# Performance work log

Hardware: AMD Instinct MI355X
Metric: run time of the kernel (lower is better)

## Reference

```python
import jax, jax.numpy as jnp
import numpy as np

HIDDEN = 1024
NUM_HEADS = 16
HEAD_DIM = HIDDEN // NUM_HEADS
B, S = 2, 2048


def setup_inputs() -> dict:
    key = jax.random.key(0)
    ks = jax.random.split(key, 7)
    scale = 1.0 / np.sqrt(HIDDEN)
    return {
        "hidden_states": jax.random.normal(ks[0], (B, S, HIDDEN), dtype=jnp.float32),
        "attention_mask": jnp.ones((B, S), dtype=jnp.float32),
        "Wq": jax.random.normal(ks[1], (HIDDEN, HIDDEN), dtype=jnp.float32) * scale,
        "bq": jax.random.normal(ks[2], (HIDDEN,), dtype=jnp.float32) * 0.02,
        "Wk": jax.random.normal(ks[3], (HIDDEN, HIDDEN), dtype=jnp.float32) * scale,
        "bk": jax.random.normal(ks[4], (HIDDEN,), dtype=jnp.float32) * 0.02,
        "Wv": jax.random.normal(ks[5], (HIDDEN, HIDDEN), dtype=jnp.float32) * scale,
        "bv": jax.random.normal(ks[6], (HIDDEN,), dtype=jnp.float32) * 0.02,
    }


def reference(hidden_states, attention_mask, Wq, bq, Wk, bk, Wv, bv):
    # Linear projections (W stored [in, out], equivalent to torch Linear).
    q = hidden_states @ Wq + bq  # [B,S,H]
    k = hidden_states @ Wk + bk
    v = hidden_states @ Wv + bv

    def split_heads(x):  # [B,S,H] -> [B,nh,S,hd]
        return x.reshape(B, S, NUM_HEADS, HEAD_DIM).transpose(0, 2, 1, 3)

    q, k, v = split_heads(q), split_heads(k), split_heads(v)

    scores = jnp.einsum("bhqd,bhkd->bhqk", q, k) / jnp.sqrt(
        jnp.asarray(HEAD_DIM, dtype=q.dtype))
    min_val = jnp.finfo(scores.dtype).min
    ext_mask = (1.0 - attention_mask[:, None, None, :]) * min_val  # [B,1,1,S]
    scores = scores + ext_mask
    probs = jax.nn.softmax(scores, axis=-1)  # eval mode: no dropout
    ctx = jnp.einsum("bhqk,bhkd->bhqd", probs, v)
    ctx = ctx.transpose(0, 2, 1, 3).reshape(B, S, HIDDEN)
    return ctx
```

## Files before the change

### kernel.cpp

```cpp
#include <hip/hip_runtime.h>
#include <hip/hip_bf16.h>
#include <cstddef>
#include <cstdint>

#define HID 1024
#define NHEADS 16
#define HDIM 64
#define BATCH 2
#define SEQ 2048
#define MROWS (BATCH * SEQ)
#define BHT (BATCH * NHEADS)

typedef __attribute__((ext_vector_type(8))) short s8v;
typedef __attribute__((ext_vector_type(4))) float f4v;
typedef __attribute__((ext_vector_type(2))) unsigned int u2v;

__device__ __forceinline__ unsigned int pkbf(float a, float b) {
    __hip_bfloat162 h = __float22bfloat162_rn(float2{a, b});
    union { __hip_bfloat162 v; unsigned int u; } c; c.v = h; return c.u;
}

__device__ __forceinline__ void lds_load16(void* lds, const void* g) {
    __builtin_amdgcn_global_load_lds(
        (const __attribute__((address_space(1))) void*)g,
        (__attribute__((address_space(3))) void*)lds, 16, 0, 0);
}

__global__ __launch_bounds__(256) void conv_fused_kernel(
    const float* __restrict__ hs, const float* __restrict__ mask,
    const float* __restrict__ Wq, const float* __restrict__ Wk,
    const float* __restrict__ Wv,
    unsigned short* __restrict__ Ah, unsigned short* __restrict__ WTh,
    float* __restrict__ lmask)
{
    if (blockIdx.x < 2048) {
        const int idx = (blockIdx.x * 256 + threadIdx.x) * 8;
        float4 v0 = *(const float4*)&hs[idx];
        float4 v1 = *(const float4*)&hs[idx + 4];
        union { unsigned int w[4]; } pk;
        pk.w[0] = pkbf(v0.x, v0.y);
        pk.w[1] = pkbf(v0.z, v0.w);
        pk.w[2] = pkbf(v1.x, v1.y);
        pk.w[3] = pkbf(v1.z, v1.w);
        *(uint4*)&Ah[idx] = *(uint4*)&pk;
    } else if (blockIdx.x < 2816) {
        const int bid = blockIdx.x - 2048;
        const int z = bid >> 8;
        const int rem = bid & 255;
        const float* W = (z == 0) ? Wq : (z == 1) ? Wk : Wv;
        unsigned short* th = WTh + (size_t)z * HID * HID;

        __shared__ float tile[64][65];
        const int t = threadIdx.x;
        const int kb = (rem >> 4) * 64, nb = (rem & 15) * 64;
        const int c4 = (t & 15) * 4;
        const int r0 = t >> 4;

#pragma unroll
        for (int i = 0; i < 4; ++i) {
            int r = r0 + i * 16;
            float4 v = *(const float4*)&W[(size_t)(kb + r) * HID + nb + c4];
            tile[r][c4 + 0] = v.x; tile[r][c4 + 1] = v.y;
            tile[r][c4 + 2] = v.z; tile[r][c4 + 3] = v.w;
        }
        __syncthreads();
#pragma unroll
        for (int i = 0; i < 4; ++i) {
            int n = r0 + i * 16;
            union { unsigned int w[2]; unsigned long long q; } pk;
            pk.w[0] = pkbf(tile[c4 + 0][n], tile[c4 + 1][n]);
            pk.w[1] = pkbf(tile[c4 + 2][n], tile[c4 + 3][n]);
            *(unsigned long long*)&th[(size_t)(nb + n) * HID + kb + c4] = pk.q;
        }
    } else {
        const int idx = (blockIdx.x - 2816) * 256 + threadIdx.x;
        lmask[idx] = (mask[idx] - 1.0f) * 1e30f;
    }
}

#define QSCALE 0.18033688011112042f

__global__ __launch_bounds__(256, 2) void qkv_mfma_kernel(
    const unsigned short* __restrict__ Ah, const unsigned short* __restrict__ WTh,
    const float* __restrict__ bq, const float* __restrict__ bk,
    const float* __restrict__ bv,
    unsigned short* __restrict__ Qg, unsigned short* __restrict__ Khi,
    unsigned short* __restrict__ VTg)
{
    __shared__ unsigned short S[24576];
    unsigned short* AS = S;
    unsigned short* B0 = S + 8192;
    unsigned short* B1 = S + 16384;

    const int z2 = blockIdx.z;
    const int t = threadIdx.x;
    const int wave = t >> 6, lane = t & 63, quad = lane >> 4, l15 = lane & 15;
    const int sw = l15 & 7;
    const int wm = wave >> 1, wn = wave & 1;
    const int rowBase = blockIdx.x * 128;
    const int colBase = blockIdx.y * 128;

    const int srow8 = lane >> 3;
    const int sc    = lane & 7;

    const unsigned short* BhQ = WTh;
    const unsigned short* BhK = WTh + (size_t)HID * HID;
    const unsigned short* BhV = WTh + (size_t)2 * HID * HID;

    size_t goffA[4], goffB[4];
#pragma unroll
    for (int it = 0; it < 4; ++it) {
        const int row = (wave * 4 + it) * 8 + srow8;
        const int gx = (sc ^ (row & 7)) * 8;
        goffA[it] = (size_t)(rowBase + row) * HID + gx;
        goffB[it] = (size_t)(colBase + row) * HID + gx;
    }

    if (z2 == 0) {
        f4v accq[4][4], acck[4][4];
#pragma unroll
        for (int mf = 0; mf < 4; ++mf)
#pragma unroll
            for (int nf = 0; nf < 4; ++nf) {
                accq[mf][nf] = (f4v){0.f, 0.f, 0.f, 0.f};
                acck[mf][nf] = (f4v){0.f, 0.f, 0.f, 0.f};
            }

        for (int kt = 0; kt < HID / 64; ++kt) {
            const int k0 = kt * 64;
            __syncthreads();
#pragma unroll
            for (int it = 0; it < 4; ++it) {
                lds_load16(&AS[(wave * 4 + it) * 512], &Ah[goffA[it] + k0]);
                lds_load16(&B0[(wave * 4 + it) * 512], &BhQ[goffB[it] + k0]);
                lds_load16(&B1[(wave * 4 + it) * 512], &BhK[goffB[it] + k0]);
            }
            __syncthreads();

#pragma unroll
            for (int kk = 0; kk < 2; ++kk) {
                const int csw = ((kk * 4 + quad) ^ sw) * 8;
                s8v af[4], bfq[4], bfk[4];
#pragma unroll
                for (int mf = 0; mf < 4; ++mf)
                    af[mf] = *(const s8v*)&AS[(wm * 64 + mf * 16 + l15) * 64 + csw];
#pragma unroll
                for (int nf = 0; nf < 4; ++nf) {
                    bfq[nf] = *(const s8v*)&B0[(wn * 64 + nf * 16 + l15) * 64 + csw];
                    bfk[nf] = *(const s8v*)&B1[(wn * 64 + nf * 16 + l15) * 64 + csw];
                }
#pragma unroll
                for (int mf = 0; mf < 4; ++mf)
#pragma unroll
                    for (int nf = 0; nf < 4; ++nf) {
                        accq[mf][nf] = __builtin_amdgcn_mfma_f32_16x16x32_bf16(bfq[nf], af[mf], accq[mf][nf], 0, 0, 0);
                        acck[mf][nf] = __builtin_amdgcn_mfma_f32_16x16x32_bf16(bfk[nf], af[mf], acck[mf][nf], 0, 0, 0);
                    }
            }
        }

#pragma unroll
        for (int nf = 0; nf < 4; ++nf) {
            const int n0 = colBase + wn * 64 + nf * 16 + quad * 4;
            const float4 bbq = *(const float4*)&bq[n0];
            const float4 bbk = *(const float4*)&bk[n0];
            const int h = n0 >> 6, d0 = n0 & 63;
#pragma unroll
            for (int mf = 0; mf < 4; ++mf) {
                const int rw = rowBase + wm * 64 + mf * 16 + l15;
                const int b = rw >> 11;
                const int ss = rw & (SEQ - 1);
                const size_t base = ((size_t)(b * NHEADS + h) * SEQ + ss) * HDIM + d0;
                union { unsigned int w[2]; unsigned long long q; } pk;
                pk.w[0] = pkbf((accq[mf][nf][0] + bbq.x) * QSCALE, (accq[mf][nf][1] + bbq.y) * QSCALE);
                pk.w[1] = pkbf((accq[mf][nf][2] + bbq.z) * QSCALE, (accq[mf][nf][3] + bbq.w) * QSCALE);
                *(unsigned long long*)&Qg[base] = pk.q;
                pk.w[0] = pkbf(acck[mf][nf][0] + bbk.x, acck[mf][nf][1] + bbk.y);
                pk.w[1] = pkbf(acck[mf][nf][2] + bbk.z, acck[mf][nf][3] + bbk.w);
                *(unsigned long long*)&Khi[base] = pk.q;
            }
        }
    } else {
        f4v acc[4][4];
#pragma unroll
        for (int mf = 0; mf < 4; ++mf)
#pragma unroll
            for (int nf = 0; nf < 4; ++nf) acc[mf][nf] = (f4v){0.f, 0.f, 0.f, 0.f};

        for (int kt = 0; kt < HID / 64; ++kt) {
            const int k0 = kt * 64;
            __syncthreads();
#pragma unroll
            for (int it = 0; it < 4; ++it) {
                lds_load16(&AS[(wave * 4 + it) * 512], &Ah[goffA[it] + k0]);
                lds_load16(&B0[(wave * 4 + it) * 512], &BhV[goffB[it] + k0]);
            }
            __syncthreads();

#pragma unroll
            for (int kk = 0; kk < 2; ++kk) {
                const int csw = ((kk * 4 + quad) ^ sw) * 8;
                s8v af[4], bf[4];
#pragma unroll
                for (int mf = 0; mf < 4; ++mf)
                    af[mf] = *(const s8v*)&AS[(wm * 64 + mf * 16 + l15) * 64 + csw];
#pragma unroll
                for (int nf = 0; nf < 4; ++nf)
                    bf[nf] = *(const s8v*)&B0[(wn * 64 + nf * 16 + l15) * 64 + csw];
#pragma unroll
                for (int mf = 0; mf < 4; ++mf)
#pragma unroll
                    for (int nf = 0; nf < 4; ++nf)
                        acc[mf][nf] = __builtin_amdgcn_mfma_f32_16x16x32_bf16(af[mf], bf[nf], acc[mf][nf], 0, 0, 0);
            }
        }

#pragma unroll
        for (int nf = 0; nf < 4; ++nf) {
            const int n = colBase + wn * 64 + nf * 16 + l15;
            const float bb = bv[n];
            const int h = n >> 6, d = n & 63;
#pragma unroll
            for (int mf = 0; mf < 4; ++mf) {
                const int rw0 = rowBase + wm * 64 + mf * 16 + quad * 4;
                const int b = rw0 >> 11;
                const int s0 = rw0 & (SEQ - 1);
                union { unsigned int w[2]; unsigned long long q; } pk;
                pk.w[0] = pkbf(acc[mf][nf][0] + bb, acc[mf][nf][1] + bb);
                pk.w[1] = pkbf(acc[mf][nf][2] + bb, acc[mf][nf][3] + bb);
                *(unsigned long long*)&VTg[((size_t)(b * NHEADS + h) * HDIM + d) * SEQ + s0] = pk.q;
            }
        }
    }
}

#define BC 64
#define NT (SEQ / BC)

#define ATTN_STEP(KT, KCUR, KNXT, VCUR, VPRV, PAOUT, PAIN, STAGEK, DOPV)      \
    do {                                                                      \
        if (STAGEK)                                                           \
            lds_load16((KNXT) + wave * 512,                                   \
                       kbase + ((KT) + 1) * BC * HDIM + koff);                \
        lds_load16((VCUR) + wave * 512, vbase + (KT) * BC + voff);            \
        float4 msv[4];                                                        \
        _Pragma("unroll") for (int mf = 0; mf < 4; ++mf)                      \
            msv[mf] = *(const float4*)&mrow[(KT) * BC + mf * 16 + quad * 4];  \
        f4v sacc[4];                                                          \
        _Pragma("unroll") for (int mf = 0; mf < 4; ++mf)                      \
            sacc[mf] = (f4v){msv[mf].x, msv[mf].y, msv[mf].z, msv[mf].w};     \
        __builtin_amdgcn_s_setprio(1);                                        \
        _Pragma("unroll") for (int mf = 0; mf < 4; ++mf) {                    \
            _Pragma("unroll") for (int ds = 0; ds < 2; ++ds) {                \
                s8v kh = *(const s8v*)&(KCUR)[(mf * 16 + l15) * HDIM +        \
                                              (((ds * 4 + quad) ^ sw) * 8)];  \
                sacc[mf] = __builtin_amdgcn_mfma_f32_16x16x32_bf16(           \
                    kh, qh[ds], sacc[mf], 0, 0, 0);                           \
            }                                                                 \
        }                                                                     \
        __builtin_amdgcn_s_setprio(0);                                        \
        unsigned int wlo[4], whi[4];                                          \
        float ps = 0.f;                                                       \
        _Pragma("unroll") for (int mf = 0; mf < 4; ++mf) {                    \
            float e0 = __builtin_amdgcn_exp2f(sacc[mf][0]);                   \
            float e1 = __builtin_amdgcn_exp2f(sacc[mf][1]);                   \
            float e2 = __builtin_amdgcn_exp2f(sacc[mf][2]);                   \
            float e3 = __builtin_amdgcn_exp2f(sacc[mf][3]);                   \
            ps += (e0 + e1) + (e2 + e3);                                      \
            wlo[mf] = pkbf(e0, e1);                                           \
            whi[mf] = pkbf(e2, e3);                                           \
        }                                                                     \
        l_r += ps;                                                            \
        _Pragma("unroll") for (int ks = 0; ks < 2; ++ks) {                    \
            unsigned int alo = wlo[ks * 2], blo = wlo[ks * 2 + 1];            \
            unsigned int ahi = whi[ks * 2], bhi = whi[ks * 2 + 1];            \
            u2v r;                                                            \
            r = __builtin_amdgcn_permlane32_swap(alo, blo, false, false);     \
            alo = r[0]; blo = r[1];                                           \
            r = __builtin_amdgcn_permlane32_swap(ahi, bhi, false, false);     \
            ahi = r[0]; bhi = r[1];                                           \
            r = __builtin_amdgcn_permlane16_swap(alo, blo, false, false);     \
            alo = r[0]; blo = r[1];                                           \
            r = __builtin_amdgcn_permlane16_swap(ahi, bhi, false, false);     \
            ahi = r[0]; bhi = r[1];                                           \
            union { unsigned int w[4]; s8v v; } up;                           \
            up.w[0] = alo; up.w[1] = ahi; up.w[2] = blo; up.w[3] = bhi;       \
            PAOUT[ks] = up.v;                                                 \
        }                                                                     \
        if (DOPV) {                                                           \
            _Pragma("unroll") for (int ks = 0; ks < 2; ++ks) {                \
                const int csw = ((ks * 4 + quad) ^ sw) * 8;                   \
                _Pragma("unroll") for (int nf = 0; nf < 4; ++nf) {            \
                    s8v vv = *(const s8v*)&(VPRV)[(nf * 16 + l15) * BC + csw];\
                    oacc[nf] = __builtin_amdgcn_mfma_f32_16x16x32_bf16(       \
                        PAIN[ks], vv, oacc[nf], 0, 0, 0);                     \
                }                                                             \
            }                                                                 \
        }                                                                     \
        __syncthreads();                                                      \
    } while (0)

__global__ __launch_bounds__(512, 4) void attn_mfma_kernel(
    const unsigned short* __restrict__ Qg, const unsigned short* __restrict__ Khi,
    const unsigned short* __restrict__ VTg,
    const float* __restrict__ lmask, float* __restrict__ out)
{
    __shared__ unsigned short Kb0[BC * HDIM];
    __shared__ unsigned short Kb1[BC * HDIM];
    __shared__ unsigned short Vb0[BC * HDIM];
    __shared__ unsigned short Vb1[BC * HDIM];

    const int t = threadIdx.x;
    const int wave = t >> 6, lane = t & 63, quad = lane >> 4, l15 = lane & 15;
    const int sw = l15 & 7;
    const int bh = blockIdx.x, b = bh >> 4, h = bh & (NHEADS - 1);
    const int qbase = blockIdx.y * 128 + wave * 16;

    const size_t hb = (size_t)bh * SEQ * HDIM;
    const unsigned short* kbase = Khi + hb;
    const unsigned short* vbase = VTg + hb;
    const float* mrow = lmask + b * SEQ;

    s8v qh[2];
#pragma unroll
    for (int ds = 0; ds < 2; ++ds) {
        size_t off = hb + (size_t)(qbase + l15) * HDIM + ds * 32 + quad * 8;
        qh[ds] = *(const s8v*)&Qg[off];
    }

    f4v oacc[4];
#pragma unroll
    for (int nf = 0; nf < 4; ++nf) oacc[nf] = (f4v){0.f, 0.f, 0.f, 0.f};
    float l_r = 0.f;

    const int srow8 = lane >> 3;
    const int sc    = lane & 7;
    const int row = wave * 8 + srow8;
    const int gx = (sc ^ (row & 7)) * 8;
    const int koff = row * HDIM + gx;
    const int voff = row * SEQ + gx;

    s8v paA[2], paB[2];

    lds_load16(&Kb0[wave * 512], kbase + koff);
    __syncthreads();

    ATTN_STEP(0, Kb0, Kb1, Vb0, Vb1, paA, paB, 1, 0);

    for (int kt = 1; kt <= 29; kt += 2) {
        ATTN_STEP(kt,     Kb1, Kb0, Vb1, Vb0, paB, paA, 1, 1);
        ATTN_STEP(kt + 1, Kb0, Kb1, Vb0, Vb1, paA, paB, 1, 1);
    }

    ATTN_STEP(31, Kb1, Kb0, Vb1, Vb0, paB, paA, 0, 1);

#pragma unroll
    for (int ks = 0; ks < 2; ++ks) {
        const int csw = ((ks * 4 + quad) ^ sw) * 8;
#pragma unroll
        for (int nf = 0; nf < 4; ++nf) {
            s8v vv = *(const s8v*)&Vb1[(nf * 16 + l15) * BC + csw];
            oacc[nf] = __builtin_amdgcn_mfma_f32_16x16x32_bf16(paB[ks], vv, oacc[nf], 0, 0, 0);
        }
    }

    {
        float v = l_r;
        v += __shfl_xor(v, 16);
        v += __shfl_xor(v, 32);
        float lv[4];
#pragma unroll
        for (int r = 0; r < 4; ++r)
            lv[r] = 1.0f / __shfl(v, quad * 4 + r);
#pragma unroll
        for (int nf = 0; nf < 4; ++nf)
#pragma unroll
            for (int r = 0; r < 4; ++r) {
                int q = qbase + quad * 4 + r;
                int d = nf * 16 + l15;
                out[((size_t)b * SEQ + q) * HID + h * HDIM + d] = oacc[nf][r] * lv[r];
            }
    }
}

extern "C" void kernel_launch(void* const* d_in, const int* in_sizes, int n_in,
                              void* d_out, int out_size, void* d_ws, size_t ws_size,
                              hipStream_t stream) {
    const float* hs   = (const float*)d_in[0];
    const float* mask = (const float*)d_in[1];
    const float* Wq   = (const float*)d_in[2];
    const float* bq   = (const float*)d_in[3];
    const float* Wk   = (const float*)d_in[4];
    const float* bk   = (const float*)d_in[5];
    const float* Wv   = (const float*)d_in[6];
    const float* bv   = (const float*)d_in[7];
    float* out = (float*)d_out;

    const size_t N = (size_t)MROWS * HID;
    unsigned short* Qg  = (unsigned short*)d_ws;
    unsigned short* Khi = Qg + N;
    unsigned short* VTg = Qg + 2 * N;
    unsigned short* Ah  = Qg + 3 * N;
    unsigned short* WTh = Qg + 4 * N;
    float* lmask = (float*)(WTh + (size_t)3 * HID * HID);

    conv_fused_kernel<<<2048 + 768 + 16, 256, 0, stream>>>(hs, mask, Wq, Wk, Wv, Ah, WTh, lmask);

    dim3 g1(MROWS / 128, HID / 128, 2);
    qkv_mfma_kernel<<<g1, 256, 0, stream>>>(Ah, WTh, bq, bk, bv, Qg, Khi, VTg);

    dim3 g2(BHT, SEQ / 128);
    attn_mfma_kernel<<<g2, 512, 0, stream>>>(Qg, Khi, VTg, lmask, out);
}
```

Baseline: 165.9 us.

## Drop LDS staging in attention; load K/V into registers with two query fragments per wave

```diff
diff --git a/kernel.cpp b/kernel.cpp
--- a/kernel.cpp
+++ b/kernel.cpp
@@ -237,148 +237,139 @@
 #define BC 64
 #define NT (SEQ / BC)
 
-#define ATTN_STEP(KT, KCUR, KNXT, VCUR, VPRV, PAOUT, PAIN, STAGEK, DOPV)      \
+#define ATTN_TILE(KT, KC, KN, MC, MN)                                         \
     do {                                                                      \
-        if (STAGEK)                                                           \
-            lds_load16((KNXT) + wave * 512,                                   \
-                       kbase + ((KT) + 1) * BC * HDIM + koff);                \
-        lds_load16((VCUR) + wave * 512, vbase + (KT) * BC + voff);            \
-        float4 msv[4];                                                        \
+        const int nt_ = ((KT) + 1) & (NT - 1);                                \
+        _Pragma("unroll") for (int mf = 0; mf < 4; ++mf) {                    \
+            _Pragma("unroll") for (int ds = 0; ds < 2; ++ds)                  \
+                KN[mf * 2 + ds] = *(const s8v*)&kbase[                        \
+                    (size_t)(nt_ * BC + mf * 16 + l15) * HDIM + ds * 32 + quad * 8]; \
+            MN[mf] = *(const float4*)&mrow[nt_ * BC + mf * 16 + quad * 4];    \
+        }                                                                     \
+        f4v sacc[2][4];                                                       \
+        _Pragma("unroll") for (int qf = 0; qf < 2; ++qf)                      \
+            _Pragma("unroll") for (int mf = 0; mf < 4; ++mf)                  \
+                sacc[qf][mf] = (f4v){MC[mf].x, MC[mf].y, MC[mf].z, MC[mf].w}; \
+        __builtin_amdgcn_s_setprio(1);                                        \
         _Pragma("unroll") for (int mf = 0; mf < 4; ++mf)                      \
-            msv[mf] = *(const float4*)&mrow[(KT) * BC + mf * 16 + quad * 4];  \
-        f4v sacc[4];                                                          \
-        _Pragma("unroll") for (int mf = 0; mf < 4; ++mf)                      \
-            sacc[mf] = (f4v){msv[mf].x, msv[mf].y, msv[mf].z, msv[mf].w};     \
-        __builtin_amdgcn_s_setprio(1);                                        \
-        _Pragma("unroll") for (int mf = 0; mf < 4; ++mf) {                    \
-            _Pragma("unroll") for (int ds = 0; ds < 2; ++ds) {                \
-                s8v kh = *(const s8v*)&(KCUR)[(mf * 16 + l15) * HDIM +        \
-                                              (((ds * 4 + quad) ^ sw) * 8)];  \
-                sacc[mf] = __builtin_amdgcn_mfma_f32_16x16x32_bf16(           \
-                    kh, qh[ds], sacc[mf], 0, 0, 0);                           \
+            _Pragma("unroll") for (int ds = 0; ds < 2; ++ds)                  \
+                _Pragma("unroll") for (int qf = 0; qf < 2; ++qf)              \
+                    sacc[qf][mf] = __builtin_amdgcn_mfma_f32_16x16x32_bf16(   \
+                        KC[mf * 2 + ds], qh[qf][ds], sacc[qf][mf], 0, 0, 0);  \
+        __builtin_amdgcn_s_setprio(0);                                        \
+        s8v vv[8];                                                            \
+        _Pragma("unroll") for (int nf = 0; nf < 4; ++nf)                      \
+            _Pragma("unroll") for (int ks = 0; ks < 2; ++ks)                  \
+                vv[nf * 2 + ks] = *(const s8v*)&vbase[                        \
+                    (size_t)(nf * 16 + l15) * SEQ + (KT) * BC + ks * 32 + quad * 8]; \
+        s8v pa[2][2];                                                         \
+        _Pragma("unroll") for (int qf = 0; qf < 2; ++qf) {                    \
+            unsigned int wlo[4], whi[4];                                      \
+            _Pragma("unroll") for (int mf = 0; mf < 4; ++mf) {                \
+                float e0 = __builtin_amdgcn_exp2f(sacc[qf][mf][0]);           \
+                float e1 = __builtin_amdgcn_exp2f(sacc[qf][mf][1]);           \
+                float e2 = __builtin_amdgcn_exp2f(sacc[qf][mf][2]);           \
+                float e3 = __builtin_amdgcn_exp2f(sacc[qf][mf][3]);           \
+                wlo[mf] = pkbf(e0, e1);                                       \
+                whi[mf] = pkbf(e2, e3);                                       \
+            }                                                                 \
+            _Pragma("unroll") for (int ks = 0; ks < 2; ++ks) {                \
+                unsigned int alo = wlo[ks * 2], blo = wlo[ks * 2 + 1];        \
+                unsigned int ahi = whi[ks * 2], bhi = whi[ks * 2 + 1];        \
+                u2v r;                                                        \
+                r = __builtin_amdgcn_permlane32_swap(alo, blo, false, false); \
+                alo = r[0]; blo = r[1];                                       \
+                r = __builtin_amdgcn_permlane32_swap(ahi, bhi, false, false); \
+                ahi = r[0]; bhi = r[1];                                       \
+                r = __builtin_amdgcn_permlane16_swap(alo, blo, false, false); \
+                alo = r[0]; blo = r[1];                                       \
+                r = __builtin_amdgcn_permlane16_swap(ahi, bhi, false, false); \
+                ahi = r[0]; bhi = r[1];                                       \
+                union { unsigned int w[4]; s8v v; } up;                       \
+                up.w[0] = alo; up.w[1] = ahi; up.w[2] = blo; up.w[3] = bhi;   \
+                pa[qf][ks] = up.v;                                            \
             }                                                                 \
         }                                                                     \
+        __builtin_amdgcn_s_setprio(1);                                        \
+        _Pragma("unroll") for (int ks = 0; ks < 2; ++ks) {                    \
+            _Pragma("unroll") for (int nf = 0; nf < 4; ++nf) {                \
+                oacc[0][nf] = __builtin_amdgcn_mfma_f32_16x16x32_bf16(        \
+                    pa[0][ks], vv[nf * 2 + ks], oacc[0][nf], 0, 0, 0);        \
+                oacc[1][nf] = __builtin_amdgcn_mfma_f32_16x16x32_bf16(        \
+                    pa[1][ks], vv[nf * 2 + ks], oacc[1][nf], 0, 0, 0);        \
+            }                                                                 \
+            lacc[0] = __builtin_amdgcn_mfma_f32_16x16x32_bf16(                \
+                pa[0][ks], ones, lacc[0], 0, 0, 0);                           \
+            lacc[1] = __builtin_amdgcn_mfma_f32_16x16x32_bf16(                \
+                pa[1][ks], ones, lacc[1], 0, 0, 0);                           \
+        }                                                                     \
         __builtin_amdgcn_s_setprio(0);                                        \
-        unsigned int wlo[4], whi[4];                                          \
-        float ps = 0.f;                                                       \
-        _Pragma("unroll") for (int mf = 0; mf < 4; ++mf) {                    \
-            float e0 = __builtin_amdgcn_exp2f(sacc[mf][0]);                   \
-            float e1 = __builtin_amdgcn_exp2f(sacc[mf][1]);                   \
-            float e2 = __builtin_amdgcn_exp2f(sacc[mf][2]);                   \
-            float e3 = __builtin_amdgcn_exp2f(sacc[mf][3]);                   \
-            ps += (e0 + e1) + (e2 + e3);                                      \
-            wlo[mf] = pkbf(e0, e1);                                           \
-            whi[mf] = pkbf(e2, e3);                                           \
-        }                                                                     \
-        l_r += ps;                                                            \
-        _Pragma("unroll") for (int ks = 0; ks < 2; ++ks) {                    \
-            unsigned int alo = wlo[ks * 2], blo = wlo[ks * 2 + 1];            \
-            unsigned int ahi = whi[ks * 2], bhi = whi[ks * 2 + 1];            \
-            u2v r;                                                            \
-            r = __builtin_amdgcn_permlane32_swap(alo, blo, false, false);     \
-            alo = r[0]; blo = r[1];                                           \
-            r = __builtin_amdgcn_permlane32_swap(ahi, bhi, false, false);     \
-            ahi = r[0]; bhi = r[1];                                           \
-            r = __builtin_amdgcn_permlane16_swap(alo, blo, false, false);     \
-            alo = r[0]; blo = r[1];                                           \
-            r = __builtin_amdgcn_permlane16_swap(ahi, bhi, false, false);     \
-            ahi = r[0]; bhi = r[1];                                           \
-            union { unsigned int w[4]; s8v v; } up;                           \
-            up.w[0] = alo; up.w[1] = ahi; up.w[2] = blo; up.w[3] = bhi;       \
-            PAOUT[ks] = up.v;                                                 \
-        }                                                                     \
-        if (DOPV) {                                                           \
-            _Pragma("unroll") for (int ks = 0; ks < 2; ++ks) {                \
-                const int csw = ((ks * 4 + quad) ^ sw) * 8;                   \
-                _Pragma("unroll") for (int nf = 0; nf < 4; ++nf) {            \
-                    s8v vv = *(const s8v*)&(VPRV)[(nf * 16 + l15) * BC + csw];\
-                    oacc[nf] = __builtin_amdgcn_mfma_f32_16x16x32_bf16(       \
-                        PAIN[ks], vv, oacc[nf], 0, 0, 0);                     \
-                }                                                             \
-            }                                                                 \
-        }                                                                     \
-        __syncthreads();                                                      \
     } while (0)
 
-__global__ __launch_bounds__(512, 4) void attn_mfma_kernel(
+__global__ __launch_bounds__(256, 2) void attn_mfma_kernel(
     const unsigned short* __restrict__ Qg, const unsigned short* __restrict__ Khi,
     const unsigned short* __restrict__ VTg,
     const float* __restrict__ lmask, float* __restrict__ out)
 {
-    __shared__ unsigned short Kb0[BC * HDIM];
-    __shared__ unsigned short Kb1[BC * HDIM];
-    __shared__ unsigned short Vb0[BC * HDIM];
-    __shared__ unsigned short Vb1[BC * HDIM];
-
     const int t = threadIdx.x;
     const int wave = t >> 6, lane = t & 63, quad = lane >> 4, l15 = lane & 15;
-    const int sw = l15 & 7;
     const int bh = blockIdx.x, b = bh >> 4, h = bh & (NHEADS - 1);
-    const int qbase = blockIdx.y * 128 + wave * 16;
+    const int qbase = blockIdx.y * 128 + wave * 32;
 
     const size_t hb = (size_t)bh * SEQ * HDIM;
     const unsigned short* kbase = Khi + hb;
     const unsigned short* vbase = VTg + hb;
     const float* mrow = lmask + b * SEQ;
 
-    s8v qh[2];
-#pragma unroll
-    for (int ds = 0; ds < 2; ++ds) {
-        size_t off = hb + (size_t)(qbase + l15) * HDIM + ds * 32 + quad * 8;
-        qh[ds] = *(const s8v*)&Qg[off];
-    }
-
-    f4v oacc[4];
-#pragma unroll
-    for (int nf = 0; nf < 4; ++nf) oacc[nf] = (f4v){0.f, 0.f, 0.f, 0.f};
-    float l_r = 0.f;
-
-    const int srow8 = lane >> 3;
-    const int sc    = lane & 7;
-    const int row = wave * 8 + srow8;
-    const int gx = (sc ^ (row & 7)) * 8;
-    const int koff = row * HDIM + gx;
-    const int voff = row * SEQ + gx;
-
-    s8v paA[2], paB[2];
-
-    lds_load16(&Kb0[wave * 512], kbase + koff);
-    __syncthreads();
-
-    ATTN_STEP(0, Kb0, Kb1, Vb0, Vb1, paA, paB, 1, 0);
-
-    for (int kt = 1; kt <= 29; kt += 2) {
-        ATTN_STEP(kt,     Kb1, Kb0, Vb1, Vb0, paB, paA, 1, 1);
-        ATTN_STEP(kt + 1, Kb0, Kb1, Vb0, Vb1, paA, paB, 1, 1);
-    }
-
-    ATTN_STEP(31, Kb1, Kb0, Vb1, Vb0, paB, paA, 0, 1);
-
-#pragma unroll
-    for (int ks = 0; ks < 2; ++ks) {
-        const int csw = ((ks * 4 + quad) ^ sw) * 8;
-#pragma unroll
-        for (int nf = 0; nf < 4; ++nf) {
-            s8v vv = *(const s8v*)&Vb1[(nf * 16 + l15) * BC + csw];
-            oacc[nf] = __builtin_amdgcn_mfma_f32_16x16x32_bf16(paB[ks], vv, oacc[nf], 0, 0, 0);
-        }
-    }
-
-    {
-        float v = l_r;
-        v += __shfl_xor(v, 16);
-        v += __shfl_xor(v, 32);
+    s8v qh[2][2];
+#pragma unroll
+    for (int qf = 0; qf < 2; ++qf)
+#pragma unroll
+        for (int ds = 0; ds < 2; ++ds) {
+            size_t off = hb + (size_t)(qbase + qf * 16 + l15) * HDIM + ds * 32 + quad * 8;
+            qh[qf][ds] = *(const s8v*)&Qg[off];
+        }
+
+    s8v ones;
+#pragma unroll
+    for (int j = 0; j < 8; ++j) ones[j] = (short)0x3F80;
+
+    f4v oacc[2][4], lacc[2];
+#pragma unroll
+    for (int qf = 0; qf < 2; ++qf) {
+#pragma unroll
+        for (int nf = 0; nf < 4; ++nf) oacc[qf][nf] = (f4v){0.f, 0.f, 0.f, 0.f};
+        lacc[qf] = (f4v){0.f, 0.f, 0.f, 0.f};
+    }
+
+    s8v kA[8], kB[8];
+    float4 mA[4], mB[4];
+#pragma unroll
+    for (int mf = 0; mf < 4; ++mf) {
+#pragma unroll
+        for (int ds = 0; ds < 2; ++ds)
+            kA[mf * 2 + ds] = *(const s8v*)&kbase[
+                (size_t)(mf * 16 + l15) * HDIM + ds * 32 + quad * 8];
+        mA[mf] = *(const float4*)&mrow[mf * 16 + quad * 4];
+    }
+
+    for (int kt = 0; kt < NT; kt += 2) {
+        ATTN_TILE(kt,     kA, kB, mA, mB);
+        ATTN_TILE(kt + 1, kB, kA, mB, mA);
+    }
+
+#pragma unroll
+    for (int qf = 0; qf < 2; ++qf) {
         float lv[4];
 #pragma unroll
-        for (int r = 0; r < 4; ++r)
-            lv[r] = 1.0f / __shfl(v, quad * 4 + r);
+        for (int r = 0; r < 4; ++r) lv[r] = 1.0f / lacc[qf][r];
 #pragma unroll
         for (int nf = 0; nf < 4; ++nf)
 #pragma unroll
             for (int r = 0; r < 4; ++r) {
-                int q = qbase + quad * 4 + r;
+                int q = qbase + qf * 16 + quad * 4 + r;
                 int d = nf * 16 + l15;
-                out[((size_t)b * SEQ + q) * HID + h * HDIM + d] = oacc[nf][r] * lv[r];
+                out[((size_t)b * SEQ + q) * HID + h * HDIM + d] = oacc[qf][nf][r] * lv[r];
             }
     }
 }
@@ -410,5 +401,5 @@
     qkv_mfma_kernel<<<g1, 256, 0, stream>>>(Ah, WTh, bq, bk, bv, Qg, Khi, VTg);
 
     dim3 g2(BHT, SEQ / 128);
-    attn_mfma_kernel<<<g2, 512, 0, stream>>>(Qg, Khi, VTg, lmask, out);
-}
+    attn_mfma_kernel<<<g2, 256, 0, stream>>>(Qg, Khi, VTg, lmask, out);
+}
```

Measured after the change: 242.6 us. 1.46x slower.
